# Kernel tuning notes

Measured on AMD Instinct MI355X. Metric: run time of the kernel, lower is better.

Reference implementation:

```python
import jax, jax.numpy as jnp
import numpy as np
from jax import lax

DIM = 64


def _dwconv(x, w, b):
    # x: [B,C,H,W], w: [C,1,kh,kw] depthwise, 'same' padding
    kh, kw = w.shape[2], w.shape[3]
    y = lax.conv_general_dilated(
        x, w, window_strides=(1, 1),
        padding=[(kh // 2, kh // 2), (kw // 2, kw // 2)],
        dimension_numbers=("NCHW", "OIHW", "NCHW"),
        feature_group_count=x.shape[1])
    return y + b[None, :, None, None]


def _conv1x1(x, w, b):
    y = lax.conv_general_dilated(
        x, w, window_strides=(1, 1), padding="VALID",
        dimension_numbers=("NCHW", "OIHW", "NCHW"))
    return y + b[None, :, None, None]


def _avgpool3(x):
    # PyTorch AvgPool2d(3,1,1) default count_include_pad=True -> sum/9
    s = lax.reduce_window(x, 0.0, lax.add, (1, 1, 3, 3), (1, 1, 1, 1),
                          [(0, 0), (0, 0), (1, 1), (1, 1)])
    return s / 9.0


def _maxpool3(x):
    return lax.reduce_window(x, -jnp.inf, lax.max, (1, 1, 3, 3), (1, 1, 1, 1),
                             [(0, 0), (0, 0), (1, 1), (1, 1)])


def setup_inputs() -> dict:
    key = jax.random.key(0)
    ks = jax.random.split(key, 18)
    C = DIM
    def w(k, shape):
        fan_in = shape[1] * shape[2] * shape[3]
        bound = 1.0 / np.sqrt(fan_in)
        return jax.random.uniform(k, shape, jnp.float32, -bound, bound)
    def b(k, fan_in):
        bound = 1.0 / np.sqrt(fan_in)
        return jax.random.uniform(k, (C,), jnp.float32, -bound, bound)
    return {
        "x": jax.random.normal(ks[0], (16, C, 128, 128), jnp.float32),
        "w55": w(ks[1], (C, 1, 5, 5)), "b55": b(ks[2], 25),
        "w17_0": w(ks[3], (C, 1, 1, 7)), "b17_0": b(ks[4], 7),
        "w17_1": w(ks[5], (C, 1, 7, 1)), "b17_1": b(ks[6], 7),
        "w111_0": w(ks[7], (C, 1, 1, 11)), "b111_0": b(ks[8], 11),
        "w111_1": w(ks[9], (C, 1, 11, 1)), "b111_1": b(ks[10], 11),
        "w211_0": w(ks[11], (C, 1, 1, 21)), "b211_0": b(ks[12], 21),
        "w211_1": w(ks[13], (C, 1, 21, 1)), "b211_1": b(ks[14], 21),
        "w11": w(ks[15], (C, C, 1, 1)), "b11": b(ks[16], C),
    }


def reference(x, w55, b55, w17_0, b17_0, w17_1, b17_1,
              w111_0, b111_0, w111_1, b111_1,
              w211_0, b211_0, w211_1, b211_1, w11, b11):
    def branch(inp):
        c55 = _dwconv(inp, w55, b55)
        c17 = _dwconv(_dwconv(inp, w17_0, b17_0), w17_1, b17_1)
        c111 = _dwconv(_dwconv(inp, w111_0, b111_0), w111_1, b111_1)
        c211 = _dwconv(_dwconv(inp, w211_0, b211_0), w211_1, b211_1)
        return _conv1x1(c55 + c17 + c111 + c211, w11, b11)

    mixer = branch(x)
    mixer_1 = branch(_avgpool3(x))
    mixer_2 = branch(_maxpool3(x))
    return (mixer + mixer_1 + mixer_2) * x
```

## Files before the change

### kernel.cpp

```cpp
#include <hip/hip_runtime.h>
#include <hip/hip_bf16.h>
#include <cstdint>

#define HH 128
#define WW 128
#define CC 64
#define BB 16
#define PLANE (HH*WW)

#define XS_OFF    0
#define XS_STR    56
#define XSTH_OFF  4704
#define H7_OFF    6000
#define H7_STR    72
#define UNION_OFF 8304
#define XRAW_STR  56
#define H11_OFF   UNION_OFF
#define H11_STR   76
#define H21_OFF   (UNION_OFF + 2432)
#define H21_STR   84
#define SMEM_FLOATS 13424

__device__ __forceinline__ float lo16(unsigned int u) {
  return __uint_as_float(u << 16);
}
__device__ __forceinline__ float hi16(unsigned int u) {
  return __uint_as_float(u & 0xffff0000u);
}

__global__ __launch_bounds__(256, 3) void k_dwsum(
    const float* __restrict__ x, float* __restrict__ T,
    const float* __restrict__ w55, const float* __restrict__ b55,
    const float* __restrict__ w17_0, const float* __restrict__ b17_0,
    const float* __restrict__ w17_1, const float* __restrict__ b17_1,
    const float* __restrict__ w111_0, const float* __restrict__ b111_0,
    const float* __restrict__ w111_1, const float* __restrict__ b111_1,
    const float* __restrict__ w211_0, const float* __restrict__ b211_0,
    const float* __restrict__ w211_1, const float* __restrict__ b211_1) {
  __shared__ float sm[SMEM_FLOATS];

  const int bid = blockIdx.x;
  const int pl = bid >> 3;
  const int t = bid & 7;
  const int tR0 = (t >> 2) * 64;
  const int tC0 = (t & 3) * 32;
  const int ch = pl & (CC - 1);
  const float* xp = x + (size_t)pl * PLANE;
  float* Tp = T + (size_t)pl * PLANE;
  const int tid = threadIdx.x;

  {
    float* xraw = sm + UNION_OFF;
    const int base_r = tR0 - 11, base_c = tC0 - 12;
    for (int i = tid; i < 86 * 14; i += 256) {
      int rr = i / 14;
      int jj = i - rr * 14;
      int gr = base_r + rr;
      int gc = base_c + jj * 4;
      float4 v = make_float4(0.f, 0.f, 0.f, 0.f);
      if ((unsigned)gr < 128u && (unsigned)gc < 128u)
        v = *(const float4*)(xp + gr * WW + gc);
      *(float4*)(xraw + rr * XRAW_STR + jj * 4) = v;
    }
  }
  __syncthreads();

  {
    const float* xraw = sm + UNION_OFF;
    __hip_bfloat16* xsTh = (__hip_bfloat16*)(sm + XSTH_OFF);
    for (int i = tid; i < 84 * 13; i += 256) {
      int rr = i % 84;
      int jj = i / 84;
      const float* rp = xraw + rr * XRAW_STR + jj * 4;
      float4 a0 = *(const float4*)(rp);
      float4 a1 = *(const float4*)(rp + 4);
      float4 b0 = *(const float4*)(rp + XRAW_STR);
      float4 b1 = *(const float4*)(rp + XRAW_STR + 4);
      float4 c0 = *(const float4*)(rp + 2 * XRAW_STR);
      float4 c1 = *(const float4*)(rp + 2 * XRAW_STR + 4);
      float w0[8] = {a0.x, a0.y, a0.z, a0.w, a1.x, a1.y, a1.z, a1.w};
      float w1[8] = {b0.x, b0.y, b0.z, b0.w, b1.x, b1.y, b1.z, b1.w};
      float w2[8] = {c0.x, c0.y, c0.z, c0.w, c1.x, c1.y, c1.z, c1.w};
      int gr = tR0 + rr - 10;
      bool rv0 = (unsigned)(gr - 1) < 128u;
      bool rv1 = (unsigned)(gr) < 128u;
      bool rv2 = (unsigned)(gr + 1) < 128u;
      int gc0 = tC0 + jj * 4 - 12;
      float M0[8], M1[8], M2[8];
      #pragma unroll
      for (int p = 1; p <= 6; ++p) {
        bool cv = (unsigned)(gc0 + p) < 128u;
        M0[p] = (rv0 && cv) ? w0[p] : -3.402823466e38f;
        M1[p] = (rv1 && cv) ? w1[p] : -3.402823466e38f;
        M2[p] = (rv2 && cv) ? w2[p] : -3.402823466e38f;
      }
      float uq[4];
      #pragma unroll
      for (int q = 0; q < 4; ++q) {
        float s = w0[q + 1] + w0[q + 2] + w0[q + 3] + w1[q + 1] + w1[q + 2] +
                  w1[q + 3] + w2[q + 1] + w2[q + 2] + w2[q + 3];
        float m = fmaxf(
            fmaxf(fmaxf(M0[q + 1], M0[q + 2]), fmaxf(M0[q + 3], M1[q + 1])),
            fmaxf(fmaxf(M1[q + 2], M1[q + 3]),
                  fmaxf(fmaxf(M2[q + 1], M2[q + 2]), M2[q + 3])));
        float val = w1[q + 2] + s * (1.f / 9.f) + m;
        bool vo = rv1 && ((unsigned)(gc0 + q + 2) < 128u);
        uq[q] = vo ? val : 0.f;
      }
      *(float4*)(sm + XS_OFF + rr * XS_STR + jj * 4) =
          make_float4(uq[0], uq[1], uq[2], uq[3]);
      int rt = rr - 8;
      if ((unsigned)rt < 68u) {
        #pragma unroll
        for (int q = 0; q < 4; ++q) {
          int ct = jj * 4 + q - 8;
          if ((unsigned)ct < 36u)
            xsTh[ct * 72 + rt] = __float2bfloat16(uq[q]);
        }
      }
    }
  }

  float k7[7], k11[11], k21[21];
  #pragma unroll
  for (int i = 0; i < 7; ++i) k7[i] = w17_0[ch * 7 + i];
  #pragma unroll
  for (int i = 0; i < 11; ++i) k11[i] = w111_0[ch * 11 + i];
  #pragma unroll
  for (int i = 0; i < 21; ++i) k21[i] = w211_0[ch * 21 + i];
  float bb7 = 3.f * b17_0[ch];
  float bb11 = 3.f * b111_0[ch];
  float bb21 = 3.f * b211_0[ch];

  __syncthreads();

  for (int it = tid; it < 84 * 4; it += 256) {
    int rr = it % 84;
    int cg = it / 84;
    float w[28];
    const float* xr = sm + XS_OFF + rr * XS_STR + cg * 8;
    #pragma unroll
    for (int j = 0; j < 7; ++j) {
      float4 v = *(const float4*)(xr + 4 * j);
      w[4 * j] = v.x; w[4 * j + 1] = v.y; w[4 * j + 2] = v.z; w[4 * j + 3] = v.w;
    }
    int gr = tR0 + rr - 10;
    bool rv = (unsigned)gr < 128u;
    bool v11r = (rr >= 5) && (rr <= 78);
    bool v7r = (rr >= 7) && (rr <= 76);
    #pragma unroll
    for (int j = 0; j < 8; ++j) {
      float a21 = bb21, a11 = bb11, a7 = bb7;
      #pragma unroll
      for (int d = 0; d < 21; ++d) a21 += k21[d] * w[j + d];
      #pragma unroll
      for (int d = 0; d < 11; ++d) a11 += k11[d] * w[j + 5 + d];
      #pragma unroll
      for (int d = 0; d < 7; ++d) a7 += k7[d] * w[j + 7 + d];
      int c = cg * 8 + j;
      sm[H21_OFF + c * H21_STR + rr] = rv ? a21 : 0.f;
      if (v11r) sm[H11_OFF + c * H11_STR + rr - 5] = rv ? a11 : 0.f;
      if (v7r) sm[H7_OFF + c * H7_STR + rr - 7] = rv ? a7 : 0.f;
    }
  }

  float v7a[7], v11a[11], v21a[21], w5a[25];
  #pragma unroll
  for (int i = 0; i < 7; ++i) v7a[i] = w17_1[ch * 7 + i];
  #pragma unroll
  for (int i = 0; i < 11; ++i) v11a[i] = w111_1[ch * 11 + i];
  #pragma unroll
  for (int i = 0; i < 21; ++i) v21a[i] = w211_1[ch * 21 + i];
  #pragma unroll
  for (int i = 0; i < 25; ++i) w5a[i] = w55[ch * 25 + i];
  float bsum = 3.f * (b55[ch] + b17_1[ch] + b111_1[ch] + b211_1[ch]);

  __syncthreads();

  {
    int c = tid & 31;
    int r0 = (tid >> 5) * 8;
    float acc[8];
    #pragma unroll
    for (int j = 0; j < 8; ++j) acc[j] = bsum;

    float A[28];
    {
      const float* hp = sm + H21_OFF + c * H21_STR + r0;
      #pragma unroll
      for (int j = 0; j < 7; ++j) {
        float4 v = *(const float4*)(hp + 4 * j);
        A[4 * j] = v.x; A[4 * j + 1] = v.y; A[4 * j + 2] = v.z; A[4 * j + 3] = v.w;
      }
      #pragma unroll
      for (int d = 0; d < 21; ++d)
        #pragma unroll
        for (int j = 0; j < 8; ++j) acc[j] += v21a[d] * A[d + j];
    }
    {
      const float* hp = sm + H11_OFF + c * H11_STR + r0;
      #pragma unroll
      for (int j = 0; j < 5; ++j) {
        float4 v = *(const float4*)(hp + 4 * j);
        A[4 * j] = v.x; A[4 * j + 1] = v.y; A[4 * j + 2] = v.z; A[4 * j + 3] = v.w;
      }
      #pragma unroll
      for (int d = 0; d < 11; ++d)
        #pragma unroll
        for (int j = 0; j < 8; ++j) acc[j] += v11a[d] * A[d + j];
    }
    {
      const float* hp = sm + H7_OFF + c * H7_STR + r0;
      #pragma unroll
      for (int j = 0; j < 4; ++j) {
        float4 v = *(const float4*)(hp + 4 * j);
        A[4 * j] = v.x; A[4 * j + 1] = v.y; A[4 * j + 2] = v.z; A[4 * j + 3] = v.w;
      }
      #pragma unroll
      for (int d = 0; d < 7; ++d)
        #pragma unroll
        for (int j = 0; j < 8; ++j) acc[j] += v7a[d] * A[d + j];
    }
    {
      const unsigned int* xp32 = (const unsigned int*)(sm + XSTH_OFF);
      #pragma unroll
      for (int dc = 0; dc < 5; ++dc) {
        const unsigned int* hp = xp32 + (((c + dc) * 72 + r0) >> 1);
        uint4 u = *(const uint4*)hp;
        uint2 u2 = *(const uint2*)(hp + 4);
        float X[12];
        X[0] = lo16(u.x);  X[1] = hi16(u.x);
        X[2] = lo16(u.y);  X[3] = hi16(u.y);
        X[4] = lo16(u.z);  X[5] = hi16(u.z);
        X[6] = lo16(u.w);  X[7] = hi16(u.w);
        X[8] = lo16(u2.x); X[9] = hi16(u2.x);
        X[10] = lo16(u2.y); X[11] = hi16(u2.y);
        #pragma unroll
        for (int dr = 0; dr < 5; ++dr)
          #pragma unroll
          for (int j = 0; j < 8; ++j) acc[j] += w5a[dr * 5 + dc] * X[j + dr];
      }
    }
    #pragma unroll
    for (int j = 0; j < 8; ++j)
      Tp[(size_t)(tR0 + r0 + j) * WW + tC0 + c] = acc[j];
  }
}

__global__ __launch_bounds__(256, 4) void k_mix(const float* __restrict__ T,
                                                const float* __restrict__ x,
                                                const float* __restrict__ w11,
                                                const float* __restrict__ b11,
                                                float* __restrict__ out) {
  __shared__ float Wt[64 * 68];
  int bid = blockIdx.x;
  int b = bid >> 7;
  int px0 = (bid & 127) * 128;
  int tid = threadIdx.x;

  for (int i = tid; i < 4096; i += 256) {
    int co = i >> 6, ci = i & 63;
    Wt[ci * 68 + co] = w11[i];
  }
  __syncthreads();

  int pxg = tid & 31;
  int cog = tid >> 5;
  const float* Tb = T + (size_t)b * (CC * PLANE) + px0 + pxg * 4;
  const float* wp = Wt + cog * 8;

  float acc[8][4];
  #pragma unroll
  for (int a = 0; a < 8; ++a)
    #pragma unroll
    for (int p = 0; p < 4; ++p) acc[a][p] = 0.f;

  float4 tb[2][4];
  #pragma unroll
  for (int kk = 0; kk < 4; ++kk)
    tb[0][kk] = *(const float4*)(Tb + (size_t)kk * PLANE);

  #pragma unroll
  for (int kc = 0; kc < 16; ++kc) {
    const int cur = kc & 1;
    if (kc < 15) {
      #pragma unroll
      for (int kk = 0; kk < 4; ++kk)
        tb[cur ^ 1][kk] =
            *(const float4*)(Tb + (size_t)((kc + 1) * 4 + kk) * PLANE);
    }
    #pragma unroll
    for (int kk = 0; kk < 4; ++kk) {
      int k = kc * 4 + kk;
      float4 q0 = *(const float4*)(wp + k * 68);
      float4 q1 = *(const float4*)(wp + k * 68 + 4);
      float wf[8] = {q0.x, q0.y, q0.z, q0.w, q1.x, q1.y, q1.z, q1.w};
      float4 tv = tb[cur][kk];
      float tvv[4] = {tv.x, tv.y, tv.z, tv.w};
      #pragma unroll
      for (int a = 0; a < 8; ++a)
        #pragma unroll
        for (int p = 0; p < 4; ++p) acc[a][p] += wf[a] * tvv[p];
    }
  }

  const float* xb = x + (size_t)b * (CC * PLANE) + px0 + pxg * 4;
  float* ob = out + (size_t)b * (CC * PLANE) + px0 + pxg * 4;
  #pragma unroll
  for (int a = 0; a < 8; ++a) {
    int co = cog * 8 + a;
    float bb = 3.f * b11[co];
    float4 xv = *(const float4*)(xb + (size_t)co * PLANE);
    float4 o;
    o.x = (acc[a][0] + bb) * xv.x;
    o.y = (acc[a][1] + bb) * xv.y;
    o.z = (acc[a][2] + bb) * xv.z;
    o.w = (acc[a][3] + bb) * xv.w;
    *(float4*)(ob + (size_t)co * PLANE) = o;
  }
}

extern "C" void kernel_launch(void* const* d_in, const int* in_sizes, int n_in,
                              void* d_out, int out_size, void* d_ws,
                              size_t ws_size, hipStream_t stream) {
  const float* x = (const float*)d_in[0];
  const float* w55 = (const float*)d_in[1];
  const float* b55 = (const float*)d_in[2];
  const float* w17_0 = (const float*)d_in[3];
  const float* b17_0 = (const float*)d_in[4];
  const float* w17_1 = (const float*)d_in[5];
  const float* b17_1 = (const float*)d_in[6];
  const float* w111_0 = (const float*)d_in[7];
  const float* b111_0 = (const float*)d_in[8];
  const float* w111_1 = (const float*)d_in[9];
  const float* b111_1 = (const float*)d_in[10];
  const float* w211_0 = (const float*)d_in[11];
  const float* b211_0 = (const float*)d_in[12];
  const float* w211_1 = (const float*)d_in[13];
  const float* b211_1 = (const float*)d_in[14];
  const float* w11 = (const float*)d_in[15];
  const float* b11 = (const float*)d_in[16];
  float* outp = (float*)d_out;

  float* T = (float*)d_ws;

  k_dwsum<<<BB * CC * 8, 256, 0, stream>>>(
      x, T, w55, b55, w17_0, b17_0, w17_1, b17_1, w111_0, b111_0, w111_1,
      b111_1, w211_0, b211_0, w211_1, b211_1);
  k_mix<<<BB * 128, 256, 0, stream>>>(T, x, w11, b11, outp);
}
```

Before: 306.6 us.

## Store intermediate column-conv results as bf16, pad T planes, deepen mix prefetch

The horizontal-conv intermediates (h7/h11/h21) are now kept in shared memory as bf16 with a common 88-element stride instead of fp32. This cuts LDS footprint (SMEM_FLOATS drops) and LDS read bandwidth in the vertical pass. The pooling prepass now has each thread produce 3 rows from 5 loaded rows, reusing the overlapping loads. The T buffer uses a padded plane stride (16512) to avoid channel aliasing in the 1x1 mix kernel, which also moves to a 3-deep prefetch with relaxed launch bounds. All of this trades some precision from bf16 rounding of the intermediates.

After: 303.1 us. About the same (-1.1%).

```diff
diff --git a/kernel.cpp b/kernel.cpp
--- a/kernel.cpp
+++ b/kernel.cpp
@@ -7,19 +7,16 @@
 #define CC 64
 #define BB 16
 #define PLANE (HH*WW)
-
-#define XS_OFF    0
-#define XS_STR    56
-#define XSTH_OFF  4704
-#define H7_OFF    6000
-#define H7_STR    72
-#define UNION_OFF 8304
-#define XRAW_STR  56
-#define H11_OFF   UNION_OFF
-#define H11_STR   76
-#define H21_OFF   (UNION_OFF + 2432)
-#define H21_STR   84
-#define SMEM_FLOATS 13424
+#define TPSTR 16512
+
+#define XS_STR    52
+#define XRAW_STR  60
+#define XSTH_H    8736
+#define H7_H      11328
+#define UNION_F   7072
+#define H11_H     14144
+#define H21_H     16960
+#define SMEM_FLOATS 12232
 
 __device__ __forceinline__ float lo16(unsigned int u) {
   return __uint_as_float(u << 16);
@@ -38,6 +35,7 @@
     const float* __restrict__ w211_0, const float* __restrict__ b211_0,
     const float* __restrict__ w211_1, const float* __restrict__ b211_1) {
   __shared__ float sm[SMEM_FLOATS];
+  __hip_bfloat16* hb = (__hip_bfloat16*)sm;
 
   const int bid = blockIdx.x;
   const int pl = bid >> 3;
@@ -46,11 +44,11 @@
   const int tC0 = (t & 3) * 32;
   const int ch = pl & (CC - 1);
   const float* xp = x + (size_t)pl * PLANE;
-  float* Tp = T + (size_t)pl * PLANE;
+  float* Tp = T + (size_t)pl * TPSTR;
   const int tid = threadIdx.x;
 
   {
-    float* xraw = sm + UNION_OFF;
+    float* xraw = sm + UNION_F;
     const int base_r = tR0 - 11, base_c = tC0 - 12;
     for (int i = tid; i < 86 * 14; i += 256) {
       int rr = i / 14;
@@ -66,56 +64,64 @@
   __syncthreads();
 
   {
-    const float* xraw = sm + UNION_OFF;
-    __hip_bfloat16* xsTh = (__hip_bfloat16*)(sm + XSTH_OFF);
-    for (int i = tid; i < 84 * 13; i += 256) {
-      int rr = i % 84;
-      int jj = i / 84;
-      const float* rp = xraw + rr * XRAW_STR + jj * 4;
-      float4 a0 = *(const float4*)(rp);
-      float4 a1 = *(const float4*)(rp + 4);
-      float4 b0 = *(const float4*)(rp + XRAW_STR);
-      float4 b1 = *(const float4*)(rp + XRAW_STR + 4);
-      float4 c0 = *(const float4*)(rp + 2 * XRAW_STR);
-      float4 c1 = *(const float4*)(rp + 2 * XRAW_STR + 4);
-      float w0[8] = {a0.x, a0.y, a0.z, a0.w, a1.x, a1.y, a1.z, a1.w};
-      float w1[8] = {b0.x, b0.y, b0.z, b0.w, b1.x, b1.y, b1.z, b1.w};
-      float w2[8] = {c0.x, c0.y, c0.z, c0.w, c1.x, c1.y, c1.z, c1.w};
-      int gr = tR0 + rr - 10;
-      bool rv0 = (unsigned)(gr - 1) < 128u;
-      bool rv1 = (unsigned)(gr) < 128u;
-      bool rv2 = (unsigned)(gr + 1) < 128u;
+    const float* xraw = sm + UNION_F;
+    __hip_bfloat16* xsTh = hb + XSTH_H;
+    for (int i = tid; i < 28 * 13; i += 256) {
+      int rg = i % 28;
+      int jj = i / 28;
+      int rr0 = rg * 3;
+      const float* rp = xraw + rr0 * XRAW_STR + jj * 4;
+      float w[5][8];
+      #pragma unroll
+      for (int k = 0; k < 5; ++k) {
+        float4 a = *(const float4*)(rp + k * XRAW_STR);
+        float4 b = *(const float4*)(rp + k * XRAW_STR + 4);
+        w[k][0] = a.x; w[k][1] = a.y; w[k][2] = a.z; w[k][3] = a.w;
+        w[k][4] = b.x; w[k][5] = b.y; w[k][6] = b.z; w[k][7] = b.w;
+      }
       int gc0 = tC0 + jj * 4 - 12;
-      float M0[8], M1[8], M2[8];
-      #pragma unroll
-      for (int p = 1; p <= 6; ++p) {
-        bool cv = (unsigned)(gc0 + p) < 128u;
-        M0[p] = (rv0 && cv) ? w0[p] : -3.402823466e38f;
-        M1[p] = (rv1 && cv) ? w1[p] : -3.402823466e38f;
-        M2[p] = (rv2 && cv) ? w2[p] : -3.402823466e38f;
-      }
-      float uq[4];
-      #pragma unroll
-      for (int q = 0; q < 4; ++q) {
-        float s = w0[q + 1] + w0[q + 2] + w0[q + 3] + w1[q + 1] + w1[q + 2] +
-                  w1[q + 3] + w2[q + 1] + w2[q + 2] + w2[q + 3];
-        float m = fmaxf(
-            fmaxf(fmaxf(M0[q + 1], M0[q + 2]), fmaxf(M0[q + 3], M1[q + 1])),
-            fmaxf(fmaxf(M1[q + 2], M1[q + 3]),
-                  fmaxf(fmaxf(M2[q + 1], M2[q + 2]), M2[q + 3])));
-        float val = w1[q + 2] + s * (1.f / 9.f) + m;
-        bool vo = rv1 && ((unsigned)(gc0 + q + 2) < 128u);
-        uq[q] = vo ? val : 0.f;
-      }
-      *(float4*)(sm + XS_OFF + rr * XS_STR + jj * 4) =
-          make_float4(uq[0], uq[1], uq[2], uq[3]);
-      int rt = rr - 8;
-      if ((unsigned)rt < 68u) {
+      bool cv[7];
+      #pragma unroll
+      for (int p = 1; p <= 6; ++p) cv[p] = (unsigned)(gc0 + p) < 128u;
+
+      #pragma unroll
+      for (int k = 0; k < 3; ++k) {
+        int rr = rr0 + k;
+        int gr = tR0 + rr - 10;
+        bool rv0 = (unsigned)(gr - 1) < 128u;
+        bool rv1 = (unsigned)(gr) < 128u;
+        bool rv2 = (unsigned)(gr + 1) < 128u;
+        float M0[7], M1[7], M2[7];
+        #pragma unroll
+        for (int p = 1; p <= 6; ++p) {
+          M0[p] = (rv0 && cv[p]) ? w[k][p] : -3.402823466e38f;
+          M1[p] = (rv1 && cv[p]) ? w[k + 1][p] : -3.402823466e38f;
+          M2[p] = (rv2 && cv[p]) ? w[k + 2][p] : -3.402823466e38f;
+        }
+        float uq[4];
         #pragma unroll
         for (int q = 0; q < 4; ++q) {
-          int ct = jj * 4 + q - 8;
-          if ((unsigned)ct < 36u)
-            xsTh[ct * 72 + rt] = __float2bfloat16(uq[q]);
+          float s = w[k][q + 1] + w[k][q + 2] + w[k][q + 3] + w[k + 1][q + 1] +
+                    w[k + 1][q + 2] + w[k + 1][q + 3] + w[k + 2][q + 1] +
+                    w[k + 2][q + 2] + w[k + 2][q + 3];
+          float m = fmaxf(
+              fmaxf(fmaxf(M0[q + 1], M0[q + 2]), fmaxf(M0[q + 3], M1[q + 1])),
+              fmaxf(fmaxf(M1[q + 2], M1[q + 3]),
+                    fmaxf(fmaxf(M2[q + 1], M2[q + 2]), M2[q + 3])));
+          float val = w[k + 1][q + 2] + s * (1.f / 9.f) + m;
+          bool vo = rv1 && ((unsigned)(gc0 + q + 2) < 128u);
+          uq[q] = vo ? val : 0.f;
+        }
+        *(float4*)(sm + rr * XS_STR + jj * 4) =
+            make_float4(uq[0], uq[1], uq[2], uq[3]);
+        int rt = rr - 8;
+        if ((unsigned)rt < 68u) {
+          #pragma unroll
+          for (int q = 0; q < 4; ++q) {
+            int ct = jj * 4 + q - 8;
+            if ((unsigned)ct < 36u)
+              xsTh[ct * 72 + rt] = __float2bfloat16(uq[q]);
+          }
         }
       }
     }
@@ -138,7 +144,7 @@
     int rr = it % 84;
     int cg = it / 84;
     float w[28];
-    const float* xr = sm + XS_OFF + rr * XS_STR + cg * 8;
+    const float* xr = sm + rr * XS_STR + cg * 8;
     #pragma unroll
     for (int j = 0; j < 7; ++j) {
       float4 v = *(const float4*)(xr + 4 * j);
@@ -158,9 +164,9 @@
       #pragma unroll
       for (int d = 0; d < 7; ++d) a7 += k7[d] * w[j + 7 + d];
       int c = cg * 8 + j;
-      sm[H21_OFF + c * H21_STR + rr] = rv ? a21 : 0.f;
-      if (v11r) sm[H11_OFF + c * H11_STR + rr - 5] = rv ? a11 : 0.f;
-      if (v7r) sm[H7_OFF + c * H7_STR + rr - 7] = rv ? a7 : 0.f;
+      hb[H21_H + c * 88 + rr] = __float2bfloat16(rv ? a21 : 0.f);
+      if (v11r) hb[H11_H + c * 88 + rr - 5] = __float2bfloat16(rv ? a11 : 0.f);
+      if (v7r) hb[H7_H + c * 88 + rr - 7] = __float2bfloat16(rv ? a7 : 0.f);
     }
   }
 
@@ -186,55 +192,61 @@
 
     float A[28];
     {
-      const float* hp = sm + H21_OFF + c * H21_STR + r0;
-      #pragma unroll
-      for (int j = 0; j < 7; ++j) {
-        float4 v = *(const float4*)(hp + 4 * j);
-        A[4 * j] = v.x; A[4 * j + 1] = v.y; A[4 * j + 2] = v.z; A[4 * j + 3] = v.w;
-      }
+      const unsigned* p = (const unsigned*)&hb[H21_H + c * 88 + r0];
+      uint4 q0 = *(const uint4*)p;
+      uint4 q1 = *(const uint4*)(p + 4);
+      uint4 q2 = *(const uint4*)(p + 8);
+      uint2 q3 = *(const uint2*)(p + 12);
+      A[0]=lo16(q0.x);A[1]=hi16(q0.x);A[2]=lo16(q0.y);A[3]=hi16(q0.y);
+      A[4]=lo16(q0.z);A[5]=hi16(q0.z);A[6]=lo16(q0.w);A[7]=hi16(q0.w);
+      A[8]=lo16(q1.x);A[9]=hi16(q1.x);A[10]=lo16(q1.y);A[11]=hi16(q1.y);
+      A[12]=lo16(q1.z);A[13]=hi16(q1.z);A[14]=lo16(q1.w);A[15]=hi16(q1.w);
+      A[16]=lo16(q2.x);A[17]=hi16(q2.x);A[18]=lo16(q2.y);A[19]=hi16(q2.y);
+      A[20]=lo16(q2.z);A[21]=hi16(q2.z);A[22]=lo16(q2.w);A[23]=hi16(q2.w);
+      A[24]=lo16(q3.x);A[25]=hi16(q3.x);A[26]=lo16(q3.y);A[27]=hi16(q3.y);
       #pragma unroll
       for (int d = 0; d < 21; ++d)
         #pragma unroll
         for (int j = 0; j < 8; ++j) acc[j] += v21a[d] * A[d + j];
     }
     {
-      const float* hp = sm + H11_OFF + c * H11_STR + r0;
-      #pragma unroll
-      for (int j = 0; j < 5; ++j) {
-        float4 v = *(const float4*)(hp + 4 * j);
-        A[4 * j] = v.x; A[4 * j + 1] = v.y; A[4 * j + 2] = v.z; A[4 * j + 3] = v.w;
-      }
+      const unsigned* p = (const unsigned*)&hb[H11_H + c * 88 + r0];
+      uint4 q0 = *(const uint4*)p;
+      uint4 q1 = *(const uint4*)(p + 4);
+      uint2 q2 = *(const uint2*)(p + 8);
+      A[0]=lo16(q0.x);A[1]=hi16(q0.x);A[2]=lo16(q0.y);A[3]=hi16(q0.y);
+      A[4]=lo16(q0.z);A[5]=hi16(q0.z);A[6]=lo16(q0.w);A[7]=hi16(q0.w);
+      A[8]=lo16(q1.x);A[9]=hi16(q1.x);A[10]=lo16(q1.y);A[11]=hi16(q1.y);
+      A[12]=lo16(q1.z);A[13]=hi16(q1.z);A[14]=lo16(q1.w);A[15]=hi16(q1.w);
+      A[16]=lo16(q2.x);A[17]=hi16(q2.x);
       #pragma unroll
       for (int d = 0; d < 11; ++d)
         #pragma unroll
         for (int j = 0; j < 8; ++j) acc[j] += v11a[d] * A[d + j];
     }
     {
-      const float* hp = sm + H7_OFF + c * H7_STR + r0;
-      #pragma unroll
-      for (int j = 0; j < 4; ++j) {
-        float4 v = *(const float4*)(hp + 4 * j);
-        A[4 * j] = v.x; A[4 * j + 1] = v.y; A[4 * j + 2] = v.z; A[4 * j + 3] = v.w;
-      }
+      const unsigned* p = (const unsigned*)&hb[H7_H + c * 88 + r0];
+      uint4 q0 = *(const uint4*)p;
+      uint4 q1 = *(const uint4*)(p + 4);
+      A[0]=lo16(q0.x);A[1]=hi16(q0.x);A[2]=lo16(q0.y);A[3]=hi16(q0.y);
+      A[4]=lo16(q0.z);A[5]=hi16(q0.z);A[6]=lo16(q0.w);A[7]=hi16(q0.w);
+      A[8]=lo16(q1.x);A[9]=hi16(q1.x);A[10]=lo16(q1.y);A[11]=hi16(q1.y);
+      A[12]=lo16(q1.z);A[13]=hi16(q1.z);
       #pragma unroll
       for (int d = 0; d < 7; ++d)
         #pragma unroll
         for (int j = 0; j < 8; ++j) acc[j] += v7a[d] * A[d + j];
     }
     {
-      const unsigned int* xp32 = (const unsigned int*)(sm + XSTH_OFF);
       #pragma unroll
       for (int dc = 0; dc < 5; ++dc) {
-        const unsigned int* hp = xp32 + (((c + dc) * 72 + r0) >> 1);
-        uint4 u = *(const uint4*)hp;
-        uint2 u2 = *(const uint2*)(hp + 4);
+        const unsigned* p = (const unsigned*)&hb[XSTH_H + (c + dc) * 72 + r0];
+        uint4 q0 = *(const uint4*)p;
+        uint2 q1 = *(const uint2*)(p + 4);
         float X[12];
-        X[0] = lo16(u.x);  X[1] = hi16(u.x);
-        X[2] = lo16(u.y);  X[3] = hi16(u.y);
-        X[4] = lo16(u.z);  X[5] = hi16(u.z);
-        X[6] = lo16(u.w);  X[7] = hi16(u.w);
-        X[8] = lo16(u2.x); X[9] = hi16(u2.x);
-        X[10] = lo16(u2.y); X[11] = hi16(u2.y);
+        X[0]=lo16(q0.x);X[1]=hi16(q0.x);X[2]=lo16(q0.y);X[3]=hi16(q0.y);
+        X[4]=lo16(q0.z);X[5]=hi16(q0.z);X[6]=lo16(q0.w);X[7]=hi16(q0.w);
+        X[8]=lo16(q1.x);X[9]=hi16(q1.x);X[10]=lo16(q1.y);X[11]=hi16(q1.y);
         #pragma unroll
         for (int dr = 0; dr < 5; ++dr)
           #pragma unroll
@@ -247,11 +259,11 @@
   }
 }
 
-__global__ __launch_bounds__(256, 4) void k_mix(const float* __restrict__ T,
-                                                const float* __restrict__ x,
-                                                const float* __restrict__ w11,
-                                                const float* __restrict__ b11,
-                                                float* __restrict__ out) {
+__global__ __launch_bounds__(256) void k_mix(const float* __restrict__ T,
+                                             const float* __restrict__ x,
+                                             const float* __restrict__ w11,
+                                             const float* __restrict__ b11,
+                                             float* __restrict__ out) {
   __shared__ float Wt[64 * 68];
   int bid = blockIdx.x;
   int b = bid >> 7;
@@ -266,7 +278,7 @@
 
   int pxg = tid & 31;
   int cog = tid >> 5;
-  const float* Tb = T + (size_t)b * (CC * PLANE) + px0 + pxg * 4;
+  const float* Tb = T + (size_t)b * 64 * TPSTR + px0 + pxg * 4;
   const float* wp = Wt + cog * 8;
 
   float acc[8][4];
@@ -275,19 +287,23 @@
     #pragma unroll
     for (int p = 0; p < 4; ++p) acc[a][p] = 0.f;
 
-  float4 tb[2][4];
+  float4 tb[3][4];
   #pragma unroll
   for (int kk = 0; kk < 4; ++kk)
-    tb[0][kk] = *(const float4*)(Tb + (size_t)kk * PLANE);
+    tb[0][kk] = *(const float4*)(Tb + (size_t)kk * TPSTR);
+  #pragma unroll
+  for (int kk = 0; kk < 4; ++kk)
+    tb[1][kk] = *(const float4*)(Tb + (size_t)(4 + kk) * TPSTR);
 
   #pragma unroll
   for (int kc = 0; kc < 16; ++kc) {
-    const int cur = kc & 1;
-    if (kc < 15) {
+    const int cur = kc % 3;
+    if (kc < 14) {
+      const int nxt = (kc + 2) % 3;
       #pragma unroll
       for (int kk = 0; kk < 4; ++kk)
-        tb[cur ^ 1][kk] =
-            *(const float4*)(Tb + (size_t)((kc + 1) * 4 + kk) * PLANE);
+        tb[nxt][kk] =
+            *(const float4*)(Tb + (size_t)((kc + 2) * 4 + kk) * TPSTR);
     }
     #pragma unroll
     for (int kk = 0; kk < 4; ++kk) {
```
